# Kernel tuning notes

Hardware: AMD Instinct MI355X
Metric: run time of the kernel (lower is better)

## Reference

```python
import jax, jax.numpy as jnp
import numpy as np

N_ITER = 2
M = 0.0
AFF_SOFTMAX = 1.0
BIG = 1e16  # finite sentinel for invalid neighbors (CUDA kernel uses inf)


def _ssn(x, s):
    B, C, H, W = x.shape
    nh, nw = H // s, W // s
    S = nh * nw
    N = H * W
    # append_grid: concat (row, col) coordinate channels scaled by M/stoken
    ii, jj = jnp.meshgrid(jnp.arange(H), jnp.arange(W), indexing='ij')
    grid = jnp.stack([ii, jj], 0).astype(x.dtype) * (M / s)  # (2,H,W)
    xg = jnp.concatenate([x, jnp.broadcast_to(grid[None], (B, 2, H, W))], 1)
    C2 = C + 2
    # adaptive_avg_pool2d with exact divisibility == block mean
    cent = xg.reshape(B, C2, nh, s, nw, s).mean(axis=(3, 5)).reshape(B, C2, S)
    # nearest-neighbor init label map (exact divisibility => i//s)
    ly = jnp.broadcast_to((jnp.arange(H) // s)[:, None], (H, W)).reshape(-1)
    lx = jnp.broadcast_to((jnp.arange(W) // s)[None, :], (H, W)).reshape(-1)
    dy = jnp.repeat(jnp.arange(-1, 2), 3)  # 9-neighborhood offsets
    dx = jnp.tile(jnp.arange(-1, 2), 3)
    ny = ly[None, :] + dy[:, None]  # (9,N)
    nx = lx[None, :] + dx[:, None]
    valid = (ny >= 0) & (ny < nh) & (nx >= 0) & (nx < nw)
    nidx = jnp.clip(ny, 0, nh - 1) * nw + jnp.clip(nx, 0, nw - 1)  # (9,N)
    pix = jnp.arange(N)
    bidx = jnp.arange(B)[:, None, None]
    px = xg.reshape(B, C2, N)
    abs_aff = None
    for k in range(N_ITER):
        cg = cent[:, :, nidx]                              # (B,C2,9,N) gather
        dist = ((px[:, :, None, :] - cg) ** 2).sum(1)      # (B,9,N)
        dist = jnp.where(valid[None], dist, BIG)
        aff = jax.nn.softmax(-AFF_SOFTMAX * dist, axis=1)  # softmax over 9 nbrs
        aff = jnp.where(valid[None], aff, 0.0)
        # sparse_coo_tensor(...).to_dense() == scatter-add into (B,S,N)
        abs_aff = jnp.zeros((B, S, N), x.dtype).at[bidx, nidx[None], pix].add(aff)
        if k < N_ITER - 1:
            num = jnp.einsum('bsn,bcn->bcs', abs_aff, px)  # weighted bmm
            den = abs_aff.sum(2)[:, None] + 1e-16
            cent = num / den
    return abs_aff, S


def setup_inputs() -> dict:
    key = jax.random.key(0)
    x = jax.random.normal(key, (4, 32, 256, 256), dtype=jnp.float32)
    return {"x": x, "stoken_size": 16}


def reference(x, stoken_size):
    return _ssn(x, int(stoken_size))
```

## Files before the change

### kernel.cpp

```cpp
#include <hip/hip_runtime.h>
#include <hip/hip_fp16.h>

#define B_  4
#define C_  32
#define W_  256
#define N_  65536
#define NH_ 16
#define S_  256
#define PADP 260
#define PADH 260
#define PSTR 304

typedef float vf4 __attribute__((ext_vector_type(4)));
typedef _Float16 h4 __attribute__((ext_vector_type(4)));

__device__ __forceinline__ float wave_sum(float v) {
    v += __shfl_down(v, 32);
    v += __shfl_down(v, 16);
    v += __shfl_down(v, 8);
    v += __shfl_down(v, 4);
    v += __shfl_down(v, 2);
    v += __shfl_down(v, 1);
    return v;
}

__device__ __forceinline__ void nt_store4(float* p, float a, float b, float c, float d) {
    vf4 v = {a, b, c, d};
    __builtin_nontemporal_store(v, (vf4*)p);
}
__device__ __forceinline__ void nt_zero4(float* p) { nt_store4(p, 0.f, 0.f, 0.f, 0.f); }

__device__ __forceinline__ void stage_tile(const float* __restrict__ x,
                                           int b, int sy, int sx, int t,
                                           float (*xsh)[PADP]) {
    const float* base = x + (size_t)b * C_ * N_ + (sy * 16) * W_ + sx * 16;
    #pragma unroll
    for (int i = 0; i < 8; ++i) {
        const int idx = i * 256 + t;
        const int c = idx >> 6, p4 = idx & 63;
        const float4 v = *(const float4*)(base + (size_t)c * N_ + (p4 >> 2) * W_ + (p4 & 3) * 4);
        *(float4*)&xsh[c][p4 * 4] = v;
    }
}

__device__ __forceinline__ void compute_aff(const float xv[C_], const float (*cl)[C_],
                                            int sy, int sx, float aff[9]) {
    float dist[9];
    #pragma unroll
    for (int k = 0; k < 9; ++k) {
        const int ny = sy + k / 3 - 1, nx = sx + k % 3 - 1;
        const bool valid = (ny >= 0) & (ny < NH_) & (nx >= 0) & (nx < NH_);
        float d = 0.f;
        #pragma unroll
        for (int c4 = 0; c4 < C_ / 4; ++c4) {
            const float4 cv = *(const float4*)&cl[k][c4 * 4];
            const float d0 = xv[c4 * 4 + 0] - cv.x;
            const float d1 = xv[c4 * 4 + 1] - cv.y;
            const float d2 = xv[c4 * 4 + 2] - cv.z;
            const float d3 = xv[c4 * 4 + 3] - cv.w;
            d += d0 * d0 + d1 * d1 + d2 * d2 + d3 * d3;
        }
        dist[k] = valid ? d : 1e30f;
    }
    float mind = dist[0];
    #pragma unroll
    for (int k = 1; k < 9; ++k) mind = fminf(mind, dist[k]);
    float sum = 0.f;
    #pragma unroll
    for (int k = 0; k < 9; ++k) {
        const float e = (dist[k] < 1e29f) ? __expf(mind - dist[k]) : 0.f;
        aff[k] = e;
        sum += e;
    }
    const float inv = 1.f / sum;
    #pragma unroll
    for (int k = 0; k < 9; ++k) aff[k] *= inv;
}

__global__ __launch_bounds__(256) void k_cent0(const float* __restrict__ x,
                                               float* __restrict__ cent0) {
    const int blk = blockIdx.x;
    const int b = blk >> 8, s = blk & 255;
    const int sy = s >> 4, sx = s & 15;
    const int t = threadIdx.x;
    const int w = t >> 6, lane = t & 63;
    const float* base = x + (size_t)b * C_ * N_ + (sy * 16) * W_ + sx * 16;
    #pragma unroll
    for (int i = 0; i < 8; ++i) {
        const int c = i * 4 + w;
        const float4 v = *(const float4*)(base + (size_t)c * N_ + (lane >> 2) * W_ + (lane & 3) * 4);
        const float sm = wave_sum(v.x + v.y + v.z + v.w);
        if (lane == 0) cent0[(size_t)blk * C_ + c] = sm * (1.0f / 256.0f);
    }
}

template <bool EXCL>
__device__ __forceinline__ void zero_strip(float* plane, int t, int r0, int r1,
                                           int sy, int sx) {
    #pragma unroll 4
    for (int i = r0; i < r1; ++i) {
        const int q = i * 256 + t;
        if (EXCL) {
            const int ty = q >> 10, tx = (q >> 2) & 15;
            if (((unsigned)(ty - sy + 1) <= 2u) & ((unsigned)(tx - sx + 1) <= 2u))
                continue;
        }
        nt_zero4(plane + q * 4);
    }
}

__global__ __launch_bounds__(256, 4) void k_part(const float* __restrict__ x,
                                                 const float* __restrict__ cent0,
                                                 float* __restrict__ part,
                                                 float* __restrict__ out) {
    const int blk = blockIdx.x;
    const int b = blk >> 8, s = blk & 255;
    const int sy = s >> 4, sx = s & 15;
    const int t = threadIdx.x;
    const int w = t >> 6, lane = t & 63;
    const bool early = (blk & 1) == 0;
    float* plane = out + ((size_t)blk << 16);
    __shared__ float cl[9][C_];
    __shared__ float xsh[C_][PADP];
    __shared__ _Float16 affs[9][PADH];
    __shared__ float lden[4][9];
    {
        const int k = t >> 5, c = t & 31;
        const int ny = sy + k / 3 - 1, nx = sx + k % 3 - 1;
        const bool valid = (ny >= 0) & (ny < NH_) & (nx >= 0) & (nx < NH_);
        cl[k][c] = valid ? cent0[(size_t)(b * S_ + ny * NH_ + nx) * C_ + c] : 0.f;
    }
    if (t < 32) {
        const int ny = sy + 1, nx = sx + 1;
        const bool valid = (ny < NH_) & (nx < NH_);
        cl[8][t] = valid ? cent0[(size_t)(b * S_ + ny * NH_ + nx) * C_ + t] : 0.f;
    }
    stage_tile(x, b, sy, sx, t, xsh);
    if (early) zero_strip<false>(plane, t, 0, 36, sy, sx);
    __syncthreads();
    float xv[C_];
    #pragma unroll
    for (int c = 0; c < C_; ++c) xv[c] = xsh[c][t];
    float aff[9];
    compute_aff(xv, cl, sy, sx, aff);
    #pragma unroll
    for (int k = 0; k < 9; ++k) {
        affs[k][t] = (_Float16)aff[k];
        const float v = wave_sum(aff[k]);
        if (lane == 0) lden[w][k] = v;
    }
    __syncthreads();
    if (!early) zero_strip<false>(plane, t, 0, 36, sy, sx);
    {
        const int k = t >> 5, c = t & 31;
        float acc = 0.f;
        #pragma unroll 4
        for (int p = 0; p < 256; p += 4) {
            const h4 a = *(const h4*)&affs[k][p];
            const float4 xc = *(const float4*)&xsh[c][p];
            acc += (float)a.x * xc.x + (float)a.y * xc.y +
                   (float)a.z * xc.z + (float)a.w * xc.w;
        }
        part[(size_t)blk * PSTR + t] = acc;
    }
    if (t < 32) {
        float acc = 0.f;
        #pragma unroll 4
        for (int p = 0; p < 256; p += 4) {
            const h4 a = *(const h4*)&affs[8][p];
            const float4 xc = *(const float4*)&xsh[t][p];
            acc += (float)a.x * xc.x + (float)a.y * xc.y +
                   (float)a.z * xc.z + (float)a.w * xc.w;
        }
        part[(size_t)blk * PSTR + 256 + t] = acc;
    }
    if (t < 9)
        part[(size_t)blk * PSTR + 288 + t] =
            lden[0][t] + lden[1][t] + lden[2][t] + lden[3][t];
}

__device__ __forceinline__ float gather_cent1(const float* __restrict__ part,
                                              int b, int ny, int nx, int c) {
    float num = 0.f, den = 0.f;
    #pragma unroll
    for (int k2 = 0; k2 < 9; ++k2) {
        const int syp = ny - (k2 / 3 - 1), sxp = nx - (k2 % 3 - 1);
        if ((syp >= 0) & (syp < NH_) & (sxp >= 0) & (sxp < NH_)) {
            const size_t base = (size_t)(b * S_ + syp * NH_ + sxp) * PSTR;
            num += part[base + k2 * 32 + c];
            den += part[base + 288 + k2];
        }
    }
    return num / (den + 1e-16f);
}

__global__ __launch_bounds__(256, 4) void k_aff9(const float* __restrict__ x,
                                                 const float* __restrict__ part,
                                                 float* __restrict__ out) {
    const int blk = blockIdx.x;
    const int b = blk >> 8, s = blk & 255;
    const int sy = s >> 4, sx = s & 15;
    const int t = threadIdx.x;
    const bool early = (blk & 1) == 0;
    float* plane = out + ((size_t)blk << 16);
    __shared__ float cl[9][C_];
    __shared__ float xsh[C_][PADP];
    __shared__ _Float16 affs[9][PADH];
    {
        const int k = t >> 5, c = t & 31;
        const int ny = sy + k / 3 - 1, nx = sx + k % 3 - 1;
        const bool valid = (ny >= 0) & (ny < NH_) & (nx >= 0) & (nx < NH_);
        cl[k][c] = valid ? gather_cent1(part, b, ny, nx, c) : 0.f;
    }
    if (t < 32) {
        const int ny = sy + 1, nx = sx + 1;
        const bool valid = (ny < NH_) & (nx < NH_);
        cl[8][t] = valid ? gather_cent1(part, b, ny, nx, t) : 0.f;
    }
    stage_tile(x, b, sy, sx, t, xsh);
    if (early) zero_strip<true>(plane, t, 36, 64, sy, sx);
    __syncthreads();
    float xv[C_];
    #pragma unroll
    for (int c = 0; c < C_; ++c) xv[c] = xsh[c][t];
    float aff[9];
    compute_aff(xv, cl, sy, sx, aff);
    #pragma unroll
    for (int k = 0; k < 9; ++k) affs[k][t] = (_Float16)aff[k];
    __syncthreads();
    if (!early) zero_strip<true>(plane, t, 36, 64, sy, sx);
    #pragma unroll
    for (int i = 0; i < 3; ++i) {
        const int idx = i * 256 + t;
        if (idx < 576) {
            const int k = idx >> 6, j4 = idx & 63;
            const int ny = sy + k / 3 - 1, nx = sx + k % 3 - 1;
            if ((ny >= 0) & (ny < NH_) & (nx >= 0) & (nx < NH_)) {
                const h4 a = *(const h4*)&affs[k][j4 * 4];
                const int gq = (sy * 16 + (j4 >> 2)) * 64 + sx * 4 + (j4 & 3);
                float* dst = out + (((size_t)(b * S_ + ny * NH_ + nx) << 16) + gq * 4);
                nt_store4(dst, (float)a.x, (float)a.y, (float)a.z, (float)a.w);
            }
        }
    }
    if ((blk | t) == 0) out[(size_t)B_ * S_ * N_] = 256.0f;
}

extern "C" void kernel_launch(void* const* d_in, const int* in_sizes, int n_in,
                              void* d_out, int out_size, void* d_ws, size_t ws_size,
                              hipStream_t stream) {
    const float* x = (const float*)d_in[0];
    float* ws = (float*)d_ws;
    float* cent0 = ws;
    float* part  = ws + 32768;
    float* out   = (float*)d_out;

    hipLaunchKernelGGL(k_cent0, dim3(B_ * S_), dim3(256), 0, stream, x, cent0);
    hipLaunchKernelGGL(k_part,  dim3(B_ * S_), dim3(256), 0, stream, x, cent0, part, out);
    hipLaunchKernelGGL(k_aff9,  dim3(B_ * S_), dim3(256), 0, stream, x, part, out);
}
```

Before: 313.2 us.

## Fuse three SSN kernels into one cooperative kernel with grid syncs

Measured after the change: 318.0 us. No clear change (+1.5%).

```diff
diff --git a/kernel.cpp b/kernel.cpp
--- a/kernel.cpp
+++ b/kernel.cpp
@@ -1,5 +1,8 @@
 #include <hip/hip_runtime.h>
 #include <hip/hip_fp16.h>
+#include <hip/hip_cooperative_groups.h>
+
+namespace cg = cooperative_groups;
 
 #define B_  4
 #define C_  32
@@ -10,6 +13,8 @@
 #define PADP 260
 #define PADH 260
 #define PSTR 304
+#define ZC_ 24
+#define ZP_ 44
 
 typedef float vf4 __attribute__((ext_vector_type(4)));
 typedef _Float16 h4 __attribute__((ext_vector_type(4)));
@@ -77,23 +82,6 @@
     for (int k = 0; k < 9; ++k) aff[k] *= inv;
 }
 
-__global__ __launch_bounds__(256) void k_cent0(const float* __restrict__ x,
-                                               float* __restrict__ cent0) {
-    const int blk = blockIdx.x;
-    const int b = blk >> 8, s = blk & 255;
-    const int sy = s >> 4, sx = s & 15;
-    const int t = threadIdx.x;
-    const int w = t >> 6, lane = t & 63;
-    const float* base = x + (size_t)b * C_ * N_ + (sy * 16) * W_ + sx * 16;
-    #pragma unroll
-    for (int i = 0; i < 8; ++i) {
-        const int c = i * 4 + w;
-        const float4 v = *(const float4*)(base + (size_t)c * N_ + (lane >> 2) * W_ + (lane & 3) * 4);
-        const float sm = wave_sum(v.x + v.y + v.z + v.w);
-        if (lane == 0) cent0[(size_t)blk * C_ + c] = sm * (1.0f / 256.0f);
-    }
-}
-
 template <bool EXCL>
 __device__ __forceinline__ void zero_strip(float* plane, int t, int r0, int r1,
                                            int sy, int sx) {
@@ -107,6 +95,44 @@
         }
         nt_zero4(plane + q * 4);
     }
+}
+
+__device__ __forceinline__ float gather_cent1(const float* __restrict__ part,
+                                              int b, int ny, int nx, int c) {
+    float num = 0.f, den = 0.f;
+    #pragma unroll
+    for (int k2 = 0; k2 < 9; ++k2) {
+        const int syp = ny - (k2 / 3 - 1), sxp = nx - (k2 % 3 - 1);
+        if ((syp >= 0) & (syp < NH_) & (sxp >= 0) & (sxp < NH_)) {
+            const size_t base = (size_t)(b * S_ + syp * NH_ + sxp) * PSTR;
+            num += part[base + k2 * 32 + c];
+            den += part[base + 288 + k2];
+        }
+    }
+    return num / (den + 1e-16f);
+}
+
+
+__global__ __launch_bounds__(256) void k_cent0(const float* __restrict__ x,
+                                               float* __restrict__ cent0,
+                                               float* __restrict__ out) {
+    const int blk = blockIdx.x;
+    const int b = blk >> 8, s = blk & 255;
+    const int sy = s >> 4, sx = s & 15;
+    const int t = threadIdx.x;
+    const int w = t >> 6, lane = t & 63;
+    const bool early = (blk & 1) == 0;
+    float* plane = out + ((size_t)blk << 16);
+    if (early) zero_strip<false>(plane, t, 0, ZC_, sy, sx);
+    const float* base = x + (size_t)b * C_ * N_ + (sy * 16) * W_ + sx * 16;
+    #pragma unroll
+    for (int i = 0; i < 8; ++i) {
+        const int c = i * 4 + w;
+        const float4 v = *(const float4*)(base + (size_t)c * N_ + (lane >> 2) * W_ + (lane & 3) * 4);
+        const float sm = wave_sum(v.x + v.y + v.z + v.w);
+        if (lane == 0) cent0[(size_t)blk * C_ + c] = sm * (1.0f / 256.0f);
+    }
+    if (!early) zero_strip<false>(plane, t, 0, ZC_, sy, sx);
 }
 
 __global__ __launch_bounds__(256, 4) void k_part(const float* __restrict__ x,
@@ -136,7 +162,7 @@
         cl[8][t] = valid ? cent0[(size_t)(b * S_ + ny * NH_ + nx) * C_ + t] : 0.f;
     }
     stage_tile(x, b, sy, sx, t, xsh);
-    if (early) zero_strip<false>(plane, t, 0, 36, sy, sx);
+    if (early) zero_strip<false>(plane, t, ZC_, ZP_, sy, sx);
     __syncthreads();
     float xv[C_];
     #pragma unroll
@@ -150,7 +176,7 @@
         if (lane == 0) lden[w][k] = v;
     }
     __syncthreads();
-    if (!early) zero_strip<false>(plane, t, 0, 36, sy, sx);
+    if (!early) zero_strip<false>(plane, t, ZC_, ZP_, sy, sx);
     {
         const int k = t >> 5, c = t & 31;
         float acc = 0.f;
@@ -177,21 +203,6 @@
     if (t < 9)
         part[(size_t)blk * PSTR + 288 + t] =
             lden[0][t] + lden[1][t] + lden[2][t] + lden[3][t];
-}
-
-__device__ __forceinline__ float gather_cent1(const float* __restrict__ part,
-                                              int b, int ny, int nx, int c) {
-    float num = 0.f, den = 0.f;
-    #pragma unroll
-    for (int k2 = 0; k2 < 9; ++k2) {
-        const int syp = ny - (k2 / 3 - 1), sxp = nx - (k2 % 3 - 1);
-        if ((syp >= 0) & (syp < NH_) & (sxp >= 0) & (sxp < NH_)) {
-            const size_t base = (size_t)(b * S_ + syp * NH_ + sxp) * PSTR;
-            num += part[base + k2 * 32 + c];
-            den += part[base + 288 + k2];
-        }
-    }
-    return num / (den + 1e-16f);
 }
 
 __global__ __launch_bounds__(256, 4) void k_aff9(const float* __restrict__ x,
@@ -218,7 +229,7 @@
         cl[8][t] = valid ? gather_cent1(part, b, ny, nx, t) : 0.f;
     }
     stage_tile(x, b, sy, sx, t, xsh);
-    if (early) zero_strip<true>(plane, t, 36, 64, sy, sx);
+    if (early) zero_strip<true>(plane, t, ZP_, 64, sy, sx);
     __syncthreads();
     float xv[C_];
     #pragma unroll
@@ -228,7 +239,7 @@
     #pragma unroll
     for (int k = 0; k < 9; ++k) affs[k][t] = (_Float16)aff[k];
     __syncthreads();
-    if (!early) zero_strip<true>(plane, t, 36, 64, sy, sx);
+    if (!early) zero_strip<true>(plane, t, ZP_, 64, sy, sx);
     #pragma unroll
     for (int i = 0; i < 3; ++i) {
         const int idx = i * 256 + t;
@@ -246,6 +257,126 @@
     if ((blk | t) == 0) out[(size_t)B_ * S_ * N_] = 256.0f;
 }
 
+__global__ __launch_bounds__(256, 4) void k_fused(const float* __restrict__ x,
+                                                  float* __restrict__ cent0,
+                                                  float* __restrict__ part,
+                                                  float* __restrict__ out) {
+    const int blk = blockIdx.x;
+    const int b = blk >> 8, s = blk & 255;
+    const int sy = s >> 4, sx = s & 15;
+    const int t = threadIdx.x;
+    const int w = t >> 6, lane = t & 63;
+    const bool early = (blk & 1) == 0;
+    float* plane = out + ((size_t)blk << 16);
+    __shared__ float cl[9][C_];
+    __shared__ float xsh[C_][PADP];
+    __shared__ _Float16 affs[9][PADH];
+    __shared__ float lden[4][9];
+
+    stage_tile(x, b, sy, sx, t, xsh);
+    if (early) zero_strip<false>(plane, t, 0, ZC_, sy, sx);
+    __syncthreads();
+    #pragma unroll
+    for (int i = 0; i < 8; ++i) {
+        const int c = i * 4 + w;
+        const float4 v = *(const float4*)&xsh[c][lane * 4];
+        const float sm = wave_sum(v.x + v.y + v.z + v.w);
+        if (lane == 0) cent0[(size_t)blk * C_ + c] = sm * (1.0f / 256.0f);
+    }
+    if (!early) zero_strip<false>(plane, t, 0, ZC_, sy, sx);
+    cg::this_grid().sync();
+
+    {
+        const int k = t >> 5, c = t & 31;
+        const int ny = sy + k / 3 - 1, nx = sx + k % 3 - 1;
+        const bool valid = (ny >= 0) & (ny < NH_) & (nx >= 0) & (nx < NH_);
+        cl[k][c] = valid ? cent0[(size_t)(b * S_ + ny * NH_ + nx) * C_ + c] : 0.f;
+    }
+    if (t < 32) {
+        const int ny = sy + 1, nx = sx + 1;
+        const bool valid = (ny < NH_) & (nx < NH_);
+        cl[8][t] = valid ? cent0[(size_t)(b * S_ + ny * NH_ + nx) * C_ + t] : 0.f;
+    }
+    if (early) zero_strip<false>(plane, t, ZC_, ZP_, sy, sx);
+    __syncthreads();
+    float xv[C_];
+    #pragma unroll
+    for (int c = 0; c < C_; ++c) xv[c] = xsh[c][t];
+    float aff[9];
+    compute_aff(xv, cl, sy, sx, aff);
+    #pragma unroll
+    for (int k = 0; k < 9; ++k) {
+        affs[k][t] = (_Float16)aff[k];
+        const float v = wave_sum(aff[k]);
+        if (lane == 0) lden[w][k] = v;
+    }
+    __syncthreads();
+    if (!early) zero_strip<false>(plane, t, ZC_, ZP_, sy, sx);
+    {
+        const int k = t >> 5, c = t & 31;
+        float acc = 0.f;
+        #pragma unroll 4
+        for (int p = 0; p < 256; p += 4) {
+            const h4 a = *(const h4*)&affs[k][p];
+            const float4 xc = *(const float4*)&xsh[c][p];
+            acc += (float)a.x * xc.x + (float)a.y * xc.y +
+                   (float)a.z * xc.z + (float)a.w * xc.w;
+        }
+        part[(size_t)blk * PSTR + t] = acc;
+    }
+    if (t < 32) {
+        float acc = 0.f;
+        #pragma unroll 4
+        for (int p = 0; p < 256; p += 4) {
+            const h4 a = *(const h4*)&affs[8][p];
+            const float4 xc = *(const float4*)&xsh[t][p];
+            acc += (float)a.x * xc.x + (float)a.y * xc.y +
+                   (float)a.z * xc.z + (float)a.w * xc.w;
+        }
+        part[(size_t)blk * PSTR + 256 + t] = acc;
+    }
+    if (t < 9)
+        part[(size_t)blk * PSTR + 288 + t] =
+            lden[0][t] + lden[1][t] + lden[2][t] + lden[3][t];
+    cg::this_grid().sync();
+
+    {
+        const int k = t >> 5, c = t & 31;
+        const int ny = sy + k / 3 - 1, nx = sx + k % 3 - 1;
+        const bool valid = (ny >= 0) & (ny < NH_) & (nx >= 0) & (nx < NH_);
+        cl[k][c] = valid ? gather_cent1(part, b, ny, nx, c) : 0.f;
+    }
+    if (t < 32) {
+        const int ny = sy + 1, nx = sx + 1;
+        const bool valid = (ny < NH_) & (nx < NH_);
+        cl[8][t] = valid ? gather_cent1(part, b, ny, nx, t) : 0.f;
+    }
+    if (early) zero_strip<true>(plane, t, ZP_, 64, sy, sx);
+    __syncthreads();
+    #pragma unroll
+    for (int c = 0; c < C_; ++c) xv[c] = xsh[c][t];
+    compute_aff(xv, cl, sy, sx, aff);
+    #pragma unroll
+    for (int k = 0; k < 9; ++k) affs[k][t] = (_Float16)aff[k];
+    __syncthreads();
+    if (!early) zero_strip<true>(plane, t, ZP_, 64, sy, sx);
+    #pragma unroll
+    for (int i = 0; i < 3; ++i) {
+        const int idx = i * 256 + t;
+        if (idx < 576) {
+            const int k = idx >> 6, j4 = idx & 63;
+            const int ny = sy + k / 3 - 1, nx = sx + k % 3 - 1;
+            if ((ny >= 0) & (ny < NH_) & (nx >= 0) & (nx < NH_)) {
+                const h4 a = *(const h4*)&affs[k][j4 * 4];
+                const int gq = (sy * 16 + (j4 >> 2)) * 64 + sx * 4 + (j4 & 3);
+                float* dst = out + (((size_t)(b * S_ + ny * NH_ + nx) << 16) + gq * 4);
+                nt_store4(dst, (float)a.x, (float)a.y, (float)a.z, (float)a.w);
+            }
+        }
+    }
+    if ((blk | t) == 0) out[(size_t)B_ * S_ * N_] = 256.0f;
+}
+
 extern "C" void kernel_launch(void* const* d_in, const int* in_sizes, int n_in,
                               void* d_out, int out_size, void* d_ws, size_t ws_size,
                               hipStream_t stream) {
@@ -255,7 +386,22 @@
     float* part  = ws + 32768;
     float* out   = (float*)d_out;
 
-    hipLaunchKernelGGL(k_cent0, dim3(B_ * S_), dim3(256), 0, stream, x, cent0);
+    static int coop_ok = -1;
+    if (coop_ok < 0) {
+        int nb = 0;
+        hipError_t e = hipOccupancyMaxActiveBlocksPerMultiprocessor(&nb, k_fused, 256, 0);
+        coop_ok = (e == hipSuccess && nb >= 4) ? 1 : 0;
+    }
+
+    if (coop_ok == 1) {
+        void* args[] = {(void*)&x, (void*)&cent0, (void*)&part, (void*)&out};
+        hipError_t e = hipLaunchCooperativeKernel((void*)k_fused, dim3(B_ * S_),
+                                                  dim3(256), args, 0, stream);
+        if (e == hipSuccess) return;
+        coop_ok = 0;
+    }
+
+    hipLaunchKernelGGL(k_cent0, dim3(B_ * S_), dim3(256), 0, stream, x, cent0, out);
     hipLaunchKernelGGL(k_part,  dim3(B_ * S_), dim3(256), 0, stream, x, cent0, part, out);
     hipLaunchKernelGGL(k_aff9,  dim3(B_ * S_), dim3(256), 0, stream, x, part, out);
 }
```
